# Kernel tuning notes

Hardware: AMD Instinct MI355X
Metric: run time of the kernel (lower is better)

## Reference

```python
import jax, jax.numpy as jnp
import numpy as np

EPS = 1e-5

def _layernorm(x, gamma, beta):
    mu = jnp.mean(x, axis=-1, keepdims=True)
    var = jnp.mean(jnp.square(x - mu), axis=-1, keepdims=True)
    return (x - mu) * jax.lax.rsqrt(var + EPS) * gamma + beta

def setup_inputs() -> dict:
    key = jax.random.key(0)
    k1, k2, k3 = jax.random.split(key, 3)
    T, B, D, H = 512, 32, 1024, 1024
    s_x = 1.0 / np.sqrt(D)
    s_h = 1.0 / np.sqrt(H)
    return {
        "input": jax.random.normal(k1, (T, B, D), dtype=jnp.float32),
        "h0": jnp.zeros((B, H), dtype=jnp.float32),
        "c0": jnp.zeros((B, H), dtype=jnp.float32),
        "Wx": jax.random.normal(k2, (4 * H, D), dtype=jnp.float32) * s_x,
        "Wh": jax.random.normal(k3, (4 * H, H), dtype=jnp.float32) * s_h,
        "gn_gamma": jnp.ones((4 * H,), dtype=jnp.float32),
        "gn_beta": jnp.zeros((4 * H,), dtype=jnp.float32),
        "cn_gamma": jnp.ones((H,), dtype=jnp.float32),
        "cn_beta": jnp.zeros((H,), dtype=jnp.float32),
    }

def reference(input, h0, c0, Wx, Wh, gn_gamma, gn_beta, cn_gamma, cn_beta):
    H = h0.shape[-1]
    # Precompute input projection for all timesteps: [T, B, 4H]
    gated_input = jnp.einsum('tbd,gd->tbg', input, Wx)

    def step(carry, gates_x):
        h, c = carry
        gates = gates_x + h @ Wh.T            # [B, 4H]
        gates = _layernorm(gates, gn_gamma, gn_beta)
        i, f, g, o = jnp.split(gates, 4, axis=1)
        c = jax.nn.sigmoid(f) * c + jax.nn.sigmoid(i) * jnp.tanh(g)
        c = _layernorm(c, cn_gamma, cn_beta)
        h = jax.nn.sigmoid(o) * jnp.tanh(c)
        return (h, c), h

    (h, c), output = jax.lax.scan(step, (h0, c0), gated_input)
    return output, h, c
```

## Files before the change

### kernel.cpp

```cpp
#include <hip/hip_runtime.h>
#include <hip/hip_bf16.h>

typedef __hip_bfloat16 bf16;
typedef __attribute__((ext_vector_type(4))) float f32x4;
typedef __attribute__((ext_vector_type(8))) short bf16x8;
typedef unsigned long long u64;
typedef unsigned short u16;
typedef unsigned u32;

#define T_STEPS 512
#define BATCH   32
#define DIM     1024
#define HID     1024
#define GATES   4096
#define NPROD   64
#define NOWN    32
#define NBLK    (NPROD + NOWN)

static __device__ __forceinline__ float sigmf(float x) {
    return 1.0f / (1.0f + __expf(-x));
}
static __device__ __forceinline__ float tanhfast(float x) {
    return 1.0f - 2.0f / (__expf(2.0f * x) + 1.0f);
}

static __device__ __forceinline__ u64 ldc_u64(const u64* p) {
    return __hip_atomic_load((u64*)p, __ATOMIC_RELAXED, __HIP_MEMORY_SCOPE_AGENT);
}
static __device__ __forceinline__ void stc_u64(u64* p, u64 v) {
    __hip_atomic_store(p, v, __ATOMIC_RELAXED, __HIP_MEMORY_SCOPE_AGENT);
}

__global__ void prep_kernel(const float* __restrict__ input,
                            const float* __restrict__ Wx,
                            const float* __restrict__ Wh,
                            const float* __restrict__ h0,
                            bf16* __restrict__ input_b,
                            bf16* __restrict__ Wx_b,
                            bf16* __restrict__ Wh_b,
                            u32* __restrict__ hx,
                            u64* __restrict__ gates_u) {
    const size_t NIN = (size_t)T_STEPS * BATCH * DIM;
    const size_t NW  = (size_t)GATES * DIM;
    const size_t NH  = (size_t)BATCH * HID;
    const size_t NG  = (size_t)BATCH * GATES;
    const size_t stride = (size_t)gridDim.x * blockDim.x;
    const size_t t0 = (size_t)blockIdx.x * blockDim.x + threadIdx.x;
    for (size_t i = t0; i < NIN; i += stride) input_b[i] = __float2bfloat16(input[i]);
    for (size_t i = t0; i < NW;  i += stride) Wx_b[i]    = __float2bfloat16(Wx[i]);
    for (size_t i = t0; i < NW;  i += stride) Wh_b[i]    = __float2bfloat16(Wh[i]);
    for (size_t i = t0; i < NH;  i += stride)
        hx[i] = (u32)__bfloat16_as_ushort(__float2bfloat16(h0[i]));
    for (size_t i = t0; i < NG;  i += stride) gates_u[i] = 0;
}

__global__ __launch_bounds__(256) void gemm_input(const bf16* __restrict__ A,
                                                  const bf16* __restrict__ W,
                                                  bf16* __restrict__ C) {
    const int bn = blockIdx.x & 31;
    const int bm = blockIdx.x >> 5;
    const int lane = threadIdx.x & 63;
    const int w = threadIdx.x >> 6;
    const int wm = (w >> 1) * 64, wn = (w & 1) * 64;
    const int lr = lane & 15;
    const int ko = (lane >> 4) * 8;

    const bf16* Abase = A + (size_t)(bm * 128 + wm + lr) * DIM + ko;
    const bf16* Wbase = W + (size_t)(bn * 128 + wn + lr) * DIM + ko;

    f32x4 acc[4][4] = {};
    for (int k = 0; k < DIM; k += 32) {
        bf16x8 af[4], bw[4];
#pragma unroll
        for (int m = 0; m < 4; ++m)
            af[m] = *(const bf16x8*)(Abase + (size_t)m * 16 * DIM + k);
#pragma unroll
        for (int n = 0; n < 4; ++n)
            bw[n] = *(const bf16x8*)(Wbase + (size_t)n * 16 * DIM + k);
#pragma unroll
        for (int m = 0; m < 4; ++m)
#pragma unroll
            for (int n = 0; n < 4; ++n)
                acc[m][n] = __builtin_amdgcn_mfma_f32_16x16x32_bf16(af[m], bw[n], acc[m][n], 0, 0, 0);
    }
    const int cr = (lane >> 4) * 4;
#pragma unroll
    for (int m = 0; m < 4; ++m)
#pragma unroll
        for (int n = 0; n < 4; ++n)
#pragma unroll
            for (int r = 0; r < 4; ++r) {
                int row = bm * 128 + wm + m * 16 + cr + r;
                int col = bn * 128 + wn + n * 16 + lr;
                C[(size_t)row * GATES + col] = __float2bfloat16(acc[m][n][r]);
            }
}

__global__ __launch_bounds__(512, 2) void scan_kernel(
    const bf16* __restrict__ gx,
    const bf16* __restrict__ Wh_b,
    const float* __restrict__ c0,
    const float* __restrict__ gn_g, const float* __restrict__ gn_b,
    const float* __restrict__ cn_g, const float* __restrict__ cn_b,
    u32* __restrict__ hx,
    u64* __restrict__ gates_u,
    float* __restrict__ out,
    float* __restrict__ h_final,
    float* __restrict__ c_final) {

    const int tid  = threadIdx.x;
    const int lane = tid & 63;
    const int w    = tid >> 6;

    if (blockIdx.x < NPROD) {
        const int mi   = blockIdx.x & 1;
        const int g    = blockIdx.x >> 1;
        const int ni   = g * 8 + w;
        const int lr   = lane & 15;
        const int hi   = lane >> 4;
        const int ko   = hi * 8;
        const int cr   = hi * 4;
        const int gcol = ni * 16 + lr;
        const int brow = mi * 16 + cr;

        __shared__ __align__(16) char hsm[16 * 2048];

        const bf16* wbase = Wh_b + (size_t)gcol * HID + ko;
        bf16x8 bfrag[32];
#pragma unroll
        for (int kk = 0; kk < 32; ++kk)
            bfrag[kk] = *(const bf16x8*)(wbase + kk * 32);

        const int arow = lr * 2048;
        const int axor = (lr & 7) << 4;

        const u16* gxp0 = (const u16*)gx + ((size_t)brow * GATES + gcol);
        u16 gxu[4];
#pragma unroll
        for (int r = 0; r < 4; ++r)
            gxu[r] = __builtin_nontemporal_load(gxp0 + (size_t)r * GATES);

        for (int t = 0; t < T_STEPS; ++t) {
            {
                const int row0 = 2 * w + (lane >> 5);
                const int l5 = lane & 31;
                const u64* hsrc = (const u64*)(hx + (size_t)(mi * 16 + row0) * HID);
                char* drow = hsm + row0 * 2048;
                const int sx = (row0 & 7) << 4;
                const u32 want = (u32)t;
                u64 vv[16];
#pragma unroll
                for (int k = 0; k < 16; ++k)
                    vv[k] = ldc_u64(hsrc + k * 32 + l5);
                for (;;) {
                    bool ok = true;
#pragma unroll
                    for (int k = 0; k < 16; ++k) {
                        if ((((u32)(vv[k] >> 16) & 0xFFFFu) != want) ||
                            ((u32)(vv[k] >> 48) != want)) {
                            ok = false;
                            vv[k] = ldc_u64(hsrc + k * 32 + l5);
                        }
                    }
                    if (ok) break;
                    __builtin_amdgcn_s_sleep(1);
                }
#pragma unroll
                for (int k = 0; k < 16; ++k) {
                    int j = k * 32 + l5;
                    u32 packed = (u32)(vv[k] & 0xFFFFu) |
                                 (((u32)(vv[k] >> 32) & 0xFFFFu) << 16);
                    *(u32*)(drow + ((4 * j) ^ sx)) = packed;
                }
            }
            __syncthreads();

            {
                f32x4 acc = {0.f, 0.f, 0.f, 0.f};
#pragma unroll
                for (int kk = 0; kk < 32; ++kk) {
                    bf16x8 a = *(const bf16x8*)(hsm + arow + ((kk * 64 + ko * 2) ^ axor));
                    acc = __builtin_amdgcn_mfma_f32_16x16x32_bf16(a, bfrag[kk], acc, 0, 0, 0);
                }
                u64* gp = gates_u + (size_t)brow * GATES + gcol;
                const u64 tagup = (u64)(u32)(t + 1) << 32;
#pragma unroll
                for (int r = 0; r < 4; ++r) {
                    union { u16 u; bf16 h; } cv; cv.u = gxu[r];
                    float val = acc[r] + __bfloat162float(cv.h);
                    stc_u64(gp + (size_t)r * GATES, tagup | (u64)__float_as_uint(val));
                }
            }

            if (t + 1 < T_STEPS) {
                const u16* gxt = gxp0 + (size_t)(t + 1) * (BATCH * GATES);
#pragma unroll
                for (int r = 0; r < 4; ++r)
                    gxu[r] = __builtin_nontemporal_load(gxt + (size_t)r * GATES);
            }
        }
        return;
    }

    const int b = blockIdx.x - NPROD;
    __shared__ float red[2][8];

    float creg[2];
#pragma unroll
    for (int q = 0; q < 2; ++q) creg[q] = c0[b * HID + 2 * tid + q];

    for (int t = 0; t < T_STEPS; ++t) {
        const u64* grow = gates_u + (size_t)b * GATES;
        const u32 want = (u32)(t + 1);
        u64 vg[4][2];
#pragma unroll
        for (int q = 0; q < 4; ++q)
#pragma unroll
            for (int e = 0; e < 2; ++e)
                vg[q][e] = ldc_u64(grow + q * 1024 + 2 * tid + e);
        for (;;) {
            bool ok = true;
#pragma unroll
            for (int q = 0; q < 4; ++q)
#pragma unroll
                for (int e = 0; e < 2; ++e)
                    if ((u32)(vg[q][e] >> 32) != want) {
                        ok = false;
                        vg[q][e] = ldc_u64(grow + q * 1024 + 2 * tid + e);
                    }
            if (ok) break;
            __builtin_amdgcn_s_sleep(1);
        }
        float gv[4][2];
        float s = 0.f, s2 = 0.f;
#pragma unroll
        for (int q = 0; q < 4; ++q)
#pragma unroll
            for (int e = 0; e < 2; ++e) {
                float x = __uint_as_float((u32)vg[q][e]);
                gv[q][e] = x;
                s += x; s2 += x * x;
            }
#pragma unroll
        for (int off = 32; off > 0; off >>= 1) {
            s  += __shfl_down(s, off, 64);
            s2 += __shfl_down(s2, off, 64);
        }
        if (lane == 0) { red[0][w] = s; red[1][w] = s2; }
        __syncthreads();
        s  = red[0][0] + red[0][1] + red[0][2] + red[0][3]
           + red[0][4] + red[0][5] + red[0][6] + red[0][7];
        s2 = red[1][0] + red[1][1] + red[1][2] + red[1][3]
           + red[1][4] + red[1][5] + red[1][6] + red[1][7];
        const float mu   = s * (1.0f / GATES);
        const float rstd = rsqrtf(s2 * (1.0f / GATES) - mu * mu + 1e-5f);

        float ov[2], cn_[2];
        float cs = 0.f, cs2 = 0.f;
#pragma unroll
        for (int q = 0; q < 2; ++q) {
            int j = 2 * tid + q;
            float iv = sigmf(   (gv[0][q] - mu) * rstd * gn_g[j]           + gn_b[j]);
            float fv = sigmf(   (gv[1][q] - mu) * rstd * gn_g[HID + j]     + gn_b[HID + j]);
            float gg = tanhfast((gv[2][q] - mu) * rstd * gn_g[2 * HID + j] + gn_b[2 * HID + j]);
            ov[q] =             (gv[3][q] - mu) * rstd * gn_g[3 * HID + j] + gn_b[3 * HID + j];
            float cnew = fv * creg[q] + iv * gg;
            cn_[q] = cnew;
            cs += cnew; cs2 += cnew * cnew;
        }
#pragma unroll
        for (int off = 32; off > 0; off >>= 1) {
            cs  += __shfl_down(cs, off, 64);
            cs2 += __shfl_down(cs2, off, 64);
        }
        __syncthreads();
        if (lane == 0) { red[0][w] = cs; red[1][w] = cs2; }
        __syncthreads();
        cs  = red[0][0] + red[0][1] + red[0][2] + red[0][3]
            + red[0][4] + red[0][5] + red[0][6] + red[0][7];
        cs2 = red[1][0] + red[1][1] + red[1][2] + red[1][3]
            + red[1][4] + red[1][5] + red[1][6] + red[1][7];
        const float mu2   = cs * (1.0f / HID);
        const float rstd2 = rsqrtf(cs2 * (1.0f / HID) - mu2 * mu2 + 1e-5f);

        float hv_[2];
        u32 he[2];
#pragma unroll
        for (int q = 0; q < 2; ++q) {
            float cn = (cn_[q] - mu2) * rstd2 * cn_g[2 * tid + q] + cn_b[2 * tid + q];
            creg[q] = cn;
            hv_[q] = sigmf(ov[q]) * tanhfast(cn);
            he[q] = ((u32)(t + 1) << 16) |
                    (u32)__bfloat16_as_ushort(__float2bfloat16(hv_[q]));
        }
        stc_u64((u64*)(hx + (size_t)b * HID + 2 * tid),
                (u64)he[0] | ((u64)he[1] << 32));

        float* orow = out + ((size_t)t * BATCH + b) * HID + 2 * tid;
#pragma unroll
        for (int q = 0; q < 2; ++q)
            __builtin_nontemporal_store(hv_[q], orow + q);
        if (t == T_STEPS - 1) {
#pragma unroll
            for (int q = 0; q < 2; ++q) {
                h_final[b * HID + 2 * tid + q] = hv_[q];
                c_final[b * HID + 2 * tid + q] = creg[q];
            }
        }
    }
}

extern "C" void kernel_launch(void* const* d_in, const int* in_sizes, int n_in,
                              void* d_out, int out_size, void* d_ws, size_t ws_size,
                              hipStream_t stream) {
    const float* input = (const float*)d_in[0];
    const float* h0    = (const float*)d_in[1];
    const float* c0    = (const float*)d_in[2];
    const float* Wx    = (const float*)d_in[3];
    const float* Wh    = (const float*)d_in[4];
    const float* gn_g  = (const float*)d_in[5];
    const float* gn_b  = (const float*)d_in[6];
    const float* cn_g  = (const float*)d_in[7];
    const float* cn_b  = (const float*)d_in[8];

    char* ws = (char*)d_ws;
    size_t off = 0;
    auto alloc = [&](size_t bytes) -> char* {
        char* p = ws + off;
        off += (bytes + 255) & ~(size_t)255;
        return p;
    };
    bf16* input_b = (bf16*)alloc((size_t)T_STEPS * BATCH * DIM * 2);
    bf16* Wx_b    = (bf16*)alloc((size_t)GATES * DIM * 2);
    bf16* Wh_b    = (bf16*)alloc((size_t)GATES * DIM * 2);
    bf16* gates_x = (bf16*)alloc((size_t)T_STEPS * BATCH * GATES * 2);
    u64*  gates_u = (u64*) alloc((size_t)BATCH * GATES * 8);
    u32*  hx      = (u32*) alloc((size_t)BATCH * HID * 4);

    float* outp    = (float*)d_out;
    float* h_final = outp + (size_t)T_STEPS * BATCH * HID;
    float* c_final = h_final + (size_t)BATCH * HID;

    hipLaunchKernelGGL(prep_kernel, dim3(2048), dim3(256), 0, stream,
                       input, Wx, Wh, h0, input_b, Wx_b, Wh_b, hx, gates_u);

    hipLaunchKernelGGL(gemm_input, dim3(4096), dim3(256), 0, stream,
                       input_b, Wx_b, gates_x);

    hipLaunchKernelGGL(scan_kernel, dim3(NBLK), dim3(512), 0, stream,
                       gates_x, Wh_b, c0, gn_g, gn_b, cn_g, cn_b,
                       hx, gates_u, outp, h_final, c_final);
}
```

Baseline: 4.120 ms.

## Use per-row sentinel flags for h and producer-side partial layernorm sums

Hidden-state exchange moves from per-element tagged u64 words to packed raw bf16 pairs guarded by one per-batch-row sentinel, which halves the polled traffic and replaces the full-tag retry loop with a single flag wait. Producer blocks now also reduce per-row sum and sum-of-squares partials for the gate layernorm and publish them tagged, so owner blocks get mean and rstd from 64 partials instead of a block-wide reduction. This removes one barrier from the owner critical path, but adds a vmcnt wait plus barrier before the sentinel store and an extra barrier in the producers.

```diff
diff --git a/kernel.cpp b/kernel.cpp
--- a/kernel.cpp
+++ b/kernel.cpp
@@ -30,6 +30,12 @@
 static __device__ __forceinline__ void stc_u64(u64* p, u64 v) {
     __hip_atomic_store(p, v, __ATOMIC_RELAXED, __HIP_MEMORY_SCOPE_AGENT);
 }
+static __device__ __forceinline__ void stc_u32(u32* p, u32 v) {
+    __hip_atomic_store(p, v, __ATOMIC_RELAXED, __HIP_MEMORY_SCOPE_AGENT);
+}
+static __device__ __forceinline__ u32 ldc_u32(const u32* p) {
+    return __hip_atomic_load((u32*)p, __ATOMIC_RELAXED, __HIP_MEMORY_SCOPE_AGENT);
+}
 
 __global__ void prep_kernel(const float* __restrict__ input,
                             const float* __restrict__ Wx,
@@ -38,20 +44,27 @@
                             bf16* __restrict__ input_b,
                             bf16* __restrict__ Wx_b,
                             bf16* __restrict__ Wh_b,
-                            u32* __restrict__ hx,
+                            u32* __restrict__ hraw,
+                            u32* __restrict__ sent,
+                            u64* __restrict__ gpart,
                             u64* __restrict__ gates_u) {
     const size_t NIN = (size_t)T_STEPS * BATCH * DIM;
     const size_t NW  = (size_t)GATES * DIM;
-    const size_t NH  = (size_t)BATCH * HID;
+    const size_t NH2 = (size_t)BATCH * 512;
     const size_t NG  = (size_t)BATCH * GATES;
     const size_t stride = (size_t)gridDim.x * blockDim.x;
     const size_t t0 = (size_t)blockIdx.x * blockDim.x + threadIdx.x;
     for (size_t i = t0; i < NIN; i += stride) input_b[i] = __float2bfloat16(input[i]);
     for (size_t i = t0; i < NW;  i += stride) Wx_b[i]    = __float2bfloat16(Wx[i]);
     for (size_t i = t0; i < NW;  i += stride) Wh_b[i]    = __float2bfloat16(Wh[i]);
-    for (size_t i = t0; i < NH;  i += stride)
-        hx[i] = (u32)__bfloat16_as_ushort(__float2bfloat16(h0[i]));
-    for (size_t i = t0; i < NG;  i += stride) gates_u[i] = 0;
+    for (size_t i = t0; i < NH2; i += stride) {
+        u32 lo = (u32)__bfloat16_as_ushort(__float2bfloat16(h0[2 * i]));
+        u32 hi = (u32)__bfloat16_as_ushort(__float2bfloat16(h0[2 * i + 1]));
+        hraw[i] = lo | (hi << 16);
+    }
+    for (size_t i = t0; i < 512;  i += stride) sent[i] = 0u;
+    for (size_t i = t0; i < 2048; i += stride) gpart[i] = 0;
+    for (size_t i = t0; i < NG;   i += stride) gates_u[i] = 0;
 }
 
 __global__ __launch_bounds__(256) void gemm_input(const bf16* __restrict__ A,
@@ -102,7 +115,9 @@
     const float* __restrict__ c0,
     const float* __restrict__ gn_g, const float* __restrict__ gn_b,
     const float* __restrict__ cn_g, const float* __restrict__ cn_b,
-    u32* __restrict__ hx,
+    u32* __restrict__ hraw,
+    u32* __restrict__ sent,
+    u64* __restrict__ gpart,
     u64* __restrict__ gates_u,
     float* __restrict__ out,
     float* __restrict__ h_final,
@@ -124,6 +139,7 @@
         const int brow = mi * 16 + cr;
 
         __shared__ __align__(16) char hsm[16 * 2048];
+        __shared__ float pr[8][16][2];
 
         const bf16* wbase = Wh_b + (size_t)gcol * HID + ko;
         bf16x8 bfrag[32];
@@ -144,37 +160,24 @@
             {
                 const int row0 = 2 * w + (lane >> 5);
                 const int l5 = lane & 31;
-                const u64* hsrc = (const u64*)(hx + (size_t)(mi * 16 + row0) * HID);
+                u32 sv = ldc_u32(sent + (mi * 16 + row0) * 16);
+                while (!__all((int)(sv >= (u32)t))) {
+                    __builtin_amdgcn_s_sleep(1);
+                    sv = ldc_u32(sent + (mi * 16 + row0) * 16);
+                }
+                const u64* hsrc = (const u64*)(hraw + (size_t)(mi * 16 + row0) * 512);
                 char* drow = hsm + row0 * 2048;
                 const int sx = (row0 & 7) << 4;
-                const u32 want = (u32)t;
-                u64 vv[16];
-#pragma unroll
-                for (int k = 0; k < 16; ++k)
-                    vv[k] = ldc_u64(hsrc + k * 32 + l5);
-                for (;;) {
-                    bool ok = true;
-#pragma unroll
-                    for (int k = 0; k < 16; ++k) {
-                        if ((((u32)(vv[k] >> 16) & 0xFFFFu) != want) ||
-                            ((u32)(vv[k] >> 48) != want)) {
-                            ok = false;
-                            vv[k] = ldc_u64(hsrc + k * 32 + l5);
-                        }
-                    }
-                    if (ok) break;
-                    __builtin_amdgcn_s_sleep(1);
+#pragma unroll
+                for (int k = 0; k < 8; ++k) {
+                    int j = k * 32 + l5;
+                    u64 v = ldc_u64(hsrc + j);
+                    *(u64*)(drow + ((8 * j) ^ sx)) = v;
                 }
-#pragma unroll
-                for (int k = 0; k < 16; ++k) {
-                    int j = k * 32 + l5;
-                    u32 packed = (u32)(vv[k] & 0xFFFFu) |
-                                 (((u32)(vv[k] >> 32) & 0xFFFFu) << 16);
-                    *(u32*)(drow + ((4 * j) ^ sx)) = packed;
-                }
             }
             __syncthreads();
 
+            float val[4];
             {
                 f32x4 acc = {0.f, 0.f, 0.f, 0.f};
 #pragma unroll
@@ -187,9 +190,37 @@
 #pragma unroll
                 for (int r = 0; r < 4; ++r) {
                     union { u16 u; bf16 h; } cv; cv.u = gxu[r];
-                    float val = acc[r] + __bfloat162float(cv.h);
-                    stc_u64(gp + (size_t)r * GATES, tagup | (u64)__float_as_uint(val));
+                    val[r] = acc[r] + __bfloat162float(cv.h);
+                    stc_u64(gp + (size_t)r * GATES, tagup | (u64)__float_as_uint(val[r]));
                 }
+            }
+
+            {
+                float s[4], q[4];
+#pragma unroll
+                for (int r = 0; r < 4; ++r) { s[r] = val[r]; q[r] = val[r] * val[r]; }
+#pragma unroll
+                for (int m = 1; m <= 8; m <<= 1)
+#pragma unroll
+                    for (int r = 0; r < 4; ++r) {
+                        s[r] += __shfl_xor(s[r], m, 64);
+                        q[r] += __shfl_xor(q[r], m, 64);
+                    }
+                if (lr == 0)
+#pragma unroll
+                    for (int r = 0; r < 4; ++r) {
+                        pr[w][cr + r][0] = s[r];
+                        pr[w][cr + r][1] = q[r];
+                    }
+            }
+            __syncthreads();
+            if (tid < 32) {
+                int row = tid >> 1, which = tid & 1;
+                float v = 0.f;
+#pragma unroll
+                for (int ww = 0; ww < 8; ++ww) v += pr[ww][row][which];
+                stc_u64(gpart + (size_t)(mi * 16 + row) * 64 + 2 * g + which,
+                        ((u64)(u32)(t + 1) << 32) | (u64)__float_as_uint(v));
             }
 
             if (t + 1 < T_STEPS) {
@@ -204,14 +235,38 @@
 
     const int b = blockIdx.x - NPROD;
     __shared__ float red[2][8];
+    __shared__ float musd[2];
 
     float creg[2];
 #pragma unroll
     for (int q = 0; q < 2; ++q) creg[q] = c0[b * HID + 2 * tid + q];
 
     for (int t = 0; t < T_STEPS; ++t) {
+        const u32 want = (u32)(t + 1);
+
+        if (w == 0) {
+            const u64* pp = gpart + (size_t)b * 64;
+            u64 pv = ldc_u64(pp + lane);
+            while (!__all((int)((u32)(pv >> 32) == want))) {
+                __builtin_amdgcn_s_sleep(1);
+                pv = ldc_u64(pp + lane);
+            }
+            float pay = __uint_as_float((u32)pv);
+            float sv = (lane & 1) ? 0.f : pay;
+            float qv = (lane & 1) ? pay : 0.f;
+#pragma unroll
+            for (int m = 1; m <= 32; m <<= 1) {
+                sv += __shfl_xor(sv, m, 64);
+                qv += __shfl_xor(qv, m, 64);
+            }
+            if (lane == 0) {
+                float mu = sv * (1.0f / GATES);
+                musd[0] = mu;
+                musd[1] = rsqrtf(qv * (1.0f / GATES) - mu * mu + 1e-5f);
+            }
+        }
+
         const u64* grow = gates_u + (size_t)b * GATES;
-        const u32 want = (u32)(t + 1);
         u64 vg[4][2];
 #pragma unroll
         for (int q = 0; q < 4; ++q)
@@ -231,40 +286,24 @@
             if (ok) break;
             __builtin_amdgcn_s_sleep(1);
         }
-        float gv[4][2];
-        float s = 0.f, s2 = 0.f;
-#pragma unroll
-        for (int q = 0; q < 4; ++q)
-#pragma unroll
-            for (int e = 0; e < 2; ++e) {
-                float x = __uint_as_float((u32)vg[q][e]);
-                gv[q][e] = x;
-                s += x; s2 += x * x;
-            }
-#pragma unroll
-        for (int off = 32; off > 0; off >>= 1) {
-            s  += __shfl_down(s, off, 64);
-            s2 += __shfl_down(s2, off, 64);
-        }
-        if (lane == 0) { red[0][w] = s; red[1][w] = s2; }
         __syncthreads();
-        s  = red[0][0] + red[0][1] + red[0][2] + red[0][3]
-           + red[0][4] + red[0][5] + red[0][6] + red[0][7];
-        s2 = red[1][0] + red[1][1] + red[1][2] + red[1][3]
-           + red[1][4] + red[1][5] + red[1][6] + red[1][7];
-        const float mu   = s * (1.0f / GATES);
-        const float rstd = rsqrtf(s2 * (1.0f / GATES) - mu * mu + 1e-5f);
+        const float mu   = musd[0];
+        const float rstd = musd[1];
 
         float ov[2], cn_[2];
         float cs = 0.f, cs2 = 0.f;
 #pragma unroll
         for (int q = 0; q < 2; ++q) {
             int j = 2 * tid + q;
-            float iv = sigmf(   (gv[0][q] - mu) * rstd * gn_g[j]           + gn_b[j]);
-            float fv = sigmf(   (gv[1][q] - mu) * rstd * gn_g[HID + j]     + gn_b[HID + j]);
-            float gg = tanhfast((gv[2][q] - mu) * rstd * gn_g[2 * HID + j] + gn_b[2 * HID + j]);
-            ov[q] =             (gv[3][q] - mu) * rstd * gn_g[3 * HID + j] + gn_b[3 * HID + j];
-            float cnew = fv * creg[q] + iv * gg;
+            float gi = __uint_as_float((u32)vg[0][q]);
+            float gf = __uint_as_float((u32)vg[1][q]);
+            float gg = __uint_as_float((u32)vg[2][q]);
+            float go = __uint_as_float((u32)vg[3][q]);
+            float iv = sigmf(   (gi - mu) * rstd * gn_g[j]           + gn_b[j]);
+            float fv = sigmf(   (gf - mu) * rstd * gn_g[HID + j]     + gn_b[HID + j]);
+            float gv = tanhfast((gg - mu) * rstd * gn_g[2 * HID + j] + gn_b[2 * HID + j]);
+            ov[q] =             (go - mu) * rstd * gn_g[3 * HID + j] + gn_b[3 * HID + j];
+            float cnew = fv * creg[q] + iv * gv;
             cn_[q] = cnew;
             cs += cnew; cs2 += cnew * cnew;
         }
@@ -273,7 +312,6 @@
             cs  += __shfl_down(cs, off, 64);
             cs2 += __shfl_down(cs2, off, 64);
         }
-        __syncthreads();
         if (lane == 0) { red[0][w] = cs; red[1][w] = cs2; }
         __syncthreads();
         cs  = red[0][0] + red[0][1] + red[0][2] + red[0][3]
@@ -284,17 +322,18 @@
         const float rstd2 = rsqrtf(cs2 * (1.0f / HID) - mu2 * mu2 + 1e-5f);
 
         float hv_[2];
-        u32 he[2];
 #pragma unroll
         for (int q = 0; q < 2; ++q) {
             float cn = (cn_[q] - mu2) * rstd2 * cn_g[2 * tid + q] + cn_b[2 * tid + q];
             creg[q] = cn;
             hv_[q] = sigmf(ov[q]) * tanhfast(cn);
-            he[q] = ((u32)(t + 1) << 16) |
-                    (u32)__bfloat16_as_ushort(__float2bfloat16(hv_[q]));
-        }
-        stc_u64((u64*)(hx + (size_t)b * HID + 2 * tid),
-                (u64)he[0] | ((u64)he[1] << 32));
+        }
+        u32 hp = (u32)__bfloat16_as_ushort(__float2bfloat16(hv_[0])) |
+                 ((u32)__bfloat16_as_ushort(__float2bfloat16(hv_[1])) << 16);
+        stc_u32(hraw + (size_t)b * 512 + tid, hp);
+        asm volatile("s_waitcnt vmcnt(0)" ::: "memory");
+        __syncthreads();
+        if (tid == 0) stc_u32(sent + b * 16, want);
 
         float* orow = out + ((size_t)t * BATCH + b) * HID + 2 * tid;
 #pragma unroll
@@ -335,19 +374,22 @@
     bf16* Wh_b    = (bf16*)alloc((size_t)GATES * DIM * 2);
     bf16* gates_x = (bf16*)alloc((size_t)T_STEPS * BATCH * GATES * 2);
     u64*  gates_u = (u64*) alloc((size_t)BATCH * GATES * 8);
-    u32*  hx      = (u32*) alloc((size_t)BATCH * HID * 4);
+    u32*  hraw    = (u32*) alloc((size_t)BATCH * 512 * 4);
+    u32*  sentb   = (u32*) alloc(512 * 4);
+    u64*  gpart   = (u64*) alloc(2048 * 8);
 
     float* outp    = (float*)d_out;
     float* h_final = outp + (size_t)T_STEPS * BATCH * HID;
     float* c_final = h_final + (size_t)BATCH * HID;
 
     hipLaunchKernelGGL(prep_kernel, dim3(2048), dim3(256), 0, stream,
-                       input, Wx, Wh, h0, input_b, Wx_b, Wh_b, hx, gates_u);
+                       input, Wx, Wh, h0, input_b, Wx_b, Wh_b,
+                       hraw, sentb, gpart, gates_u);
 
     hipLaunchKernelGGL(gemm_input, dim3(4096), dim3(256), 0, stream,
                        input_b, Wx_b, gates_x);
 
     hipLaunchKernelGGL(scan_kernel, dim3(NBLK), dim3(512), 0, stream,
                        gates_x, Wh_b, c0, gn_g, gn_b, cn_g, cn_b,
-                       hx, gates_u, outp, h_final, c_final);
-}
+                       hraw, sentb, gpart, gates_u, outp, h_final, c_final);
+}
```

New measurement: 4.591 ms. +11.4%, slower.

## Fuse input-projection GEMM into the persistent scan kernel with per-tile ready flags

Applied to the files above, without the earlier changes.

Removes the separate bf16 conversion pass and the standalone input GEMM. The GEMM now runs as extra blocks inside the scan launch, converting fp32 to bf16 on the fly and writing a transposed gate buffer. Scan producer blocks spin on per-tile flags before reading each timestep's input gates, so the projection overlaps the recurrence. The risks are deadlock or slowdown if GEMM blocks are not co-resident or are scheduled after the scan blocks, and extra contention from the GEMM blocks sharing CUs with the latency-critical scan.

```diff
diff --git a/kernel.cpp b/kernel.cpp
--- a/kernel.cpp
+++ b/kernel.cpp
@@ -15,7 +15,11 @@
 #define GATES   4096
 #define NPROD   64
 #define NOWN    32
-#define NBLK    (NPROD + NOWN)
+#define NSCAN   (NPROD + NOWN)
+#define MTILES  128
+#define NTILES  16
+#define NGEMM   (MTILES * NTILES)
+#define MAGIC   0x5EED0001u
 
 static __device__ __forceinline__ float sigmf(float x) {
     return 1.0f / (1.0f + __expf(-x));
@@ -30,80 +34,50 @@
 static __device__ __forceinline__ void stc_u64(u64* p, u64 v) {
     __hip_atomic_store(p, v, __ATOMIC_RELAXED, __HIP_MEMORY_SCOPE_AGENT);
 }
-
-__global__ void prep_kernel(const float* __restrict__ input,
-                            const float* __restrict__ Wx,
-                            const float* __restrict__ Wh,
-                            const float* __restrict__ h0,
-                            bf16* __restrict__ input_b,
-                            bf16* __restrict__ Wx_b,
-                            bf16* __restrict__ Wh_b,
-                            u32* __restrict__ hx,
-                            u64* __restrict__ gates_u) {
-    const size_t NIN = (size_t)T_STEPS * BATCH * DIM;
-    const size_t NW  = (size_t)GATES * DIM;
-    const size_t NH  = (size_t)BATCH * HID;
-    const size_t NG  = (size_t)BATCH * GATES;
+static __device__ __forceinline__ void stc_u32(u32* p, u32 v) {
+    __hip_atomic_store(p, v, __ATOMIC_RELAXED, __HIP_MEMORY_SCOPE_AGENT);
+}
+static __device__ __forceinline__ u32 ldc_u32(const u32* p) {
+    return __hip_atomic_load((u32*)p, __ATOMIC_RELAXED, __HIP_MEMORY_SCOPE_AGENT);
+}
+
+static __device__ __forceinline__ bf16x8 cvt8(const float* p) {
+    float4 x = *(const float4*)p;
+    float4 y = *(const float4*)(p + 4);
+    bf16x8 r;
+    ((u16*)&r)[0] = __bfloat16_as_ushort(__float2bfloat16(x.x));
+    ((u16*)&r)[1] = __bfloat16_as_ushort(__float2bfloat16(x.y));
+    ((u16*)&r)[2] = __bfloat16_as_ushort(__float2bfloat16(x.z));
+    ((u16*)&r)[3] = __bfloat16_as_ushort(__float2bfloat16(x.w));
+    ((u16*)&r)[4] = __bfloat16_as_ushort(__float2bfloat16(y.x));
+    ((u16*)&r)[5] = __bfloat16_as_ushort(__float2bfloat16(y.y));
+    ((u16*)&r)[6] = __bfloat16_as_ushort(__float2bfloat16(y.z));
+    ((u16*)&r)[7] = __bfloat16_as_ushort(__float2bfloat16(y.w));
+    return r;
+}
+
+__global__ void init_kernel(u32* __restrict__ hx,
+                            u64* __restrict__ gates_u,
+                            u32* __restrict__ gxsent) {
     const size_t stride = (size_t)gridDim.x * blockDim.x;
     const size_t t0 = (size_t)blockIdx.x * blockDim.x + threadIdx.x;
-    for (size_t i = t0; i < NIN; i += stride) input_b[i] = __float2bfloat16(input[i]);
-    for (size_t i = t0; i < NW;  i += stride) Wx_b[i]    = __float2bfloat16(Wx[i]);
-    for (size_t i = t0; i < NW;  i += stride) Wh_b[i]    = __float2bfloat16(Wh[i]);
-    for (size_t i = t0; i < NH;  i += stride)
-        hx[i] = (u32)__bfloat16_as_ushort(__float2bfloat16(h0[i]));
-    for (size_t i = t0; i < NG;  i += stride) gates_u[i] = 0;
-}
-
-__global__ __launch_bounds__(256) void gemm_input(const bf16* __restrict__ A,
-                                                  const bf16* __restrict__ W,
-                                                  bf16* __restrict__ C) {
-    const int bn = blockIdx.x & 31;
-    const int bm = blockIdx.x >> 5;
-    const int lane = threadIdx.x & 63;
-    const int w = threadIdx.x >> 6;
-    const int wm = (w >> 1) * 64, wn = (w & 1) * 64;
-    const int lr = lane & 15;
-    const int ko = (lane >> 4) * 8;
-
-    const bf16* Abase = A + (size_t)(bm * 128 + wm + lr) * DIM + ko;
-    const bf16* Wbase = W + (size_t)(bn * 128 + wn + lr) * DIM + ko;
-
-    f32x4 acc[4][4] = {};
-    for (int k = 0; k < DIM; k += 32) {
-        bf16x8 af[4], bw[4];
-#pragma unroll
-        for (int m = 0; m < 4; ++m)
-            af[m] = *(const bf16x8*)(Abase + (size_t)m * 16 * DIM + k);
-#pragma unroll
-        for (int n = 0; n < 4; ++n)
-            bw[n] = *(const bf16x8*)(Wbase + (size_t)n * 16 * DIM + k);
-#pragma unroll
-        for (int m = 0; m < 4; ++m)
-#pragma unroll
-            for (int n = 0; n < 4; ++n)
-                acc[m][n] = __builtin_amdgcn_mfma_f32_16x16x32_bf16(af[m], bw[n], acc[m][n], 0, 0, 0);
-    }
-    const int cr = (lane >> 4) * 4;
-#pragma unroll
-    for (int m = 0; m < 4; ++m)
-#pragma unroll
-        for (int n = 0; n < 4; ++n)
-#pragma unroll
-            for (int r = 0; r < 4; ++r) {
-                int row = bm * 128 + wm + m * 16 + cr + r;
-                int col = bn * 128 + wn + n * 16 + lr;
-                C[(size_t)row * GATES + col] = __float2bfloat16(acc[m][n][r]);
-            }
-}
-
-__global__ __launch_bounds__(512, 2) void scan_kernel(
-    const bf16* __restrict__ gx,
-    const bf16* __restrict__ Wh_b,
+    for (size_t i = t0; i < (size_t)BATCH * HID; i += stride) hx[i] = 0xFFFFFFFFu;
+    for (size_t i = t0; i < (size_t)BATCH * GATES; i += stride) gates_u[i] = 0;
+    for (size_t i = t0; i < (size_t)MTILES * NTILES; i += stride) gxsent[i] = 0u;
+}
+
+__global__ __launch_bounds__(512, 2) void fused_kernel(
+    const float* __restrict__ input,
+    const float* __restrict__ Wx,
+    const float* __restrict__ Wh,
+    const float* __restrict__ h0,
     const float* __restrict__ c0,
     const float* __restrict__ gn_g, const float* __restrict__ gn_b,
     const float* __restrict__ cn_g, const float* __restrict__ cn_b,
     u32* __restrict__ hx,
     u64* __restrict__ gates_u,
+    bf16* __restrict__ gxT,
+    u32* __restrict__ gxsent,
     float* __restrict__ out,
     float* __restrict__ h_final,
     float* __restrict__ c_final) {
@@ -111,6 +85,52 @@
     const int tid  = threadIdx.x;
     const int lane = tid & 63;
     const int w    = tid >> 6;
+
+    if (blockIdx.x >= NSCAN) {
+        const int gid = blockIdx.x - NSCAN;
+        const int bm = gid >> 4;
+        const int bn = gid & 15;
+        const int wm = (w >> 2) * 64, wn = (w & 3) * 64;
+        const int lr = lane & 15;
+        const int ko = (lane >> 4) * 8;
+
+        const float* Af = input + (size_t)(bm * 128 + wm + lr) * DIM + ko;
+        const float* Bf = Wx    + (size_t)(bn * 256 + wn + lr) * DIM + ko;
+
+        f32x4 acc[4][4] = {};
+        for (int k = 0; k < DIM; k += 32) {
+            bf16x8 af[4], bw[4];
+#pragma unroll
+            for (int m = 0; m < 4; ++m)
+                af[m] = cvt8(Af + (size_t)m * 16 * DIM + k);
+#pragma unroll
+            for (int n = 0; n < 4; ++n)
+                bw[n] = cvt8(Bf + (size_t)n * 16 * DIM + k);
+#pragma unroll
+            for (int m = 0; m < 4; ++m)
+#pragma unroll
+                for (int n = 0; n < 4; ++n)
+                    acc[m][n] = __builtin_amdgcn_mfma_f32_16x16x32_bf16(af[m], bw[n], acc[m][n], 0, 0, 0);
+        }
+        const int cr = (lane >> 4) * 4;
+        u64* gxT64 = (u64*)gxT;
+#pragma unroll
+        for (int m = 0; m < 4; ++m)
+#pragma unroll
+            for (int n = 0; n < 4; ++n) {
+                int col = bn * 256 + wn + n * 16 + lr;
+                int rb  = bm * 128 + wm + m * 16 + cr;
+                u64 pk = 0;
+#pragma unroll
+                for (int r = 0; r < 4; ++r)
+                    pk |= (u64)__bfloat16_as_ushort(__float2bfloat16(acc[m][n][r])) << (16 * r);
+                stc_u64(gxT64 + (size_t)col * 4096 + (rb >> 2), pk);
+            }
+        asm volatile("s_waitcnt vmcnt(0)" ::: "memory");
+        __syncthreads();
+        if (tid == 0) stc_u32(gxsent + bm * NTILES + bn, MAGIC);
+        return;
+    }
 
     if (blockIdx.x < NPROD) {
         const int mi   = blockIdx.x & 1;
@@ -125,20 +145,29 @@
 
         __shared__ __align__(16) char hsm[16 * 2048];
 
-        const bf16* wbase = Wh_b + (size_t)gcol * HID + ko;
+        const float* wf = Wh + (size_t)gcol * DIM + ko;
         bf16x8 bfrag[32];
 #pragma unroll
         for (int kk = 0; kk < 32; ++kk)
-            bfrag[kk] = *(const bf16x8*)(wbase + kk * 32);
+            bfrag[kk] = cvt8(wf + kk * 32);
 
         const int arow = lr * 2048;
         const int axor = (lr & 7) << 4;
 
-        const u16* gxp0 = (const u16*)gx + ((size_t)brow * GATES + gcol);
+        const u64* gxT64 = (const u64*)gxT;
+        const int ntile = g >> 1;
         u16 gxu[4];
-#pragma unroll
-        for (int r = 0; r < 4; ++r)
-            gxu[r] = __builtin_nontemporal_load(gxp0 + (size_t)r * GATES);
+        {
+            int mtile = (2 * 0 + mi) >> 3;
+            u32 sv = ldc_u32(gxsent + mtile * NTILES + ntile);
+            while (sv != MAGIC) {
+                __builtin_amdgcn_s_sleep(2);
+                sv = ldc_u32(gxsent + mtile * NTILES + ntile);
+            }
+            u64 v = ldc_u64(gxT64 + (size_t)gcol * 4096 + 0 * 8 + mi * 4 + hi);
+            gxu[0] = (u16)v; gxu[1] = (u16)(v >> 16);
+            gxu[2] = (u16)(v >> 32); gxu[3] = (u16)(v >> 48);
+        }
 
         for (int t = 0; t < T_STEPS; ++t) {
             {
@@ -193,10 +222,16 @@
             }
 
             if (t + 1 < T_STEPS) {
-                const u16* gxt = gxp0 + (size_t)(t + 1) * (BATCH * GATES);
-#pragma unroll
-                for (int r = 0; r < 4; ++r)
-                    gxu[r] = __builtin_nontemporal_load(gxt + (size_t)r * GATES);
+                int tn = t + 1;
+                int mtile = (2 * tn + mi) >> 3;
+                u32 sv = ldc_u32(gxsent + mtile * NTILES + ntile);
+                while (sv != MAGIC) {
+                    __builtin_amdgcn_s_sleep(2);
+                    sv = ldc_u32(gxsent + mtile * NTILES + ntile);
+                }
+                u64 v = ldc_u64(gxT64 + (size_t)gcol * 4096 + tn * 8 + mi * 4 + hi);
+                gxu[0] = (u16)v; gxu[1] = (u16)(v >> 16);
+                gxu[2] = (u16)(v >> 32); gxu[3] = (u16)(v >> 48);
             }
         }
         return;
@@ -208,6 +243,12 @@
     float creg[2];
 #pragma unroll
     for (int q = 0; q < 2; ++q) creg[q] = c0[b * HID + 2 * tid + q];
+
+    {
+        u32 e0 = (u32)__bfloat16_as_ushort(__float2bfloat16(h0[b * HID + 2 * tid]));
+        u32 e1 = (u32)__bfloat16_as_ushort(__float2bfloat16(h0[b * HID + 2 * tid + 1]));
+        stc_u64((u64*)(hx + (size_t)b * HID + 2 * tid), (u64)e0 | ((u64)e1 << 32));
+    }
 
     for (int t = 0; t < T_STEPS; ++t) {
         const u64* grow = gates_u + (size_t)b * GATES;
@@ -330,24 +371,19 @@
         off += (bytes + 255) & ~(size_t)255;
         return p;
     };
-    bf16* input_b = (bf16*)alloc((size_t)T_STEPS * BATCH * DIM * 2);
-    bf16* Wx_b    = (bf16*)alloc((size_t)GATES * DIM * 2);
-    bf16* Wh_b    = (bf16*)alloc((size_t)GATES * DIM * 2);
-    bf16* gates_x = (bf16*)alloc((size_t)T_STEPS * BATCH * GATES * 2);
     u64*  gates_u = (u64*) alloc((size_t)BATCH * GATES * 8);
     u32*  hx      = (u32*) alloc((size_t)BATCH * HID * 4);
+    u32*  gxsent  = (u32*) alloc((size_t)MTILES * NTILES * 4);
+    bf16* gxT     = (bf16*)alloc((size_t)GATES * (T_STEPS * BATCH) * 2);
 
     float* outp    = (float*)d_out;
     float* h_final = outp + (size_t)T_STEPS * BATCH * HID;
     float* c_final = h_final + (size_t)BATCH * HID;
 
-    hipLaunchKernelGGL(prep_kernel, dim3(2048), dim3(256), 0, stream,
-                       input, Wx, Wh, h0, input_b, Wx_b, Wh_b, hx, gates_u);
-
-    hipLaunchKernelGGL(gemm_input, dim3(4096), dim3(256), 0, stream,
-                       input_b, Wx_b, gates_x);
-
-    hipLaunchKernelGGL(scan_kernel, dim3(NBLK), dim3(512), 0, stream,
-                       gates_x, Wh_b, c0, gn_g, gn_b, cn_g, cn_b,
-                       hx, gates_u, outp, h_final, c_final);
-}
+    hipLaunchKernelGGL(init_kernel, dim3(256), dim3(256), 0, stream,
+                       hx, gates_u, gxsent);
+
+    hipLaunchKernelGGL(fused_kernel, dim3(NSCAN + NGEMM), dim3(512), 0, stream,
+                       input, Wx, Wh, h0, c0, gn_g, gn_b, cn_g, cn_b,
+                       hx, gates_u, gxT, gxsent, outp, h_final, c_final);
+}
```

New measurement: 3.818 ms. -7.3%, faster.
